# Performance work log

Hardware: AMD Instinct MI355X
Metric: run time of the kernel (lower is better)

Reference implementation:

```python
import jax, jax.numpy as jnp
import numpy as np

T, S, N, E, H, FF = 1024, 2048, 4, 1024, 16, 4096
HD = E // H
EPS = 1e-5


def layer_norm(x, g, b):
    mu = jnp.mean(x, axis=-1, keepdims=True)
    var = jnp.mean(jnp.square(x - mu), axis=-1, keepdims=True)
    return (x - mu) / jnp.sqrt(var + EPS) * g + b


def mha(q_in, k_in, v_in, w_in, b_in, w_out, b_out):
    # q_in: (T,N,E), k_in/v_in: (S,N,E); matches torch F.linear with (3E,E) weight
    t, n, e = q_in.shape
    s = k_in.shape[0]
    wq, wk, wv = jnp.split(w_in, 3, axis=0)
    bq, bk, bv = jnp.split(b_in, 3)
    q = (q_in @ wq.T + bq) * (HD ** -0.5)
    k = k_in @ wk.T + bk
    v = v_in @ wv.T + bv
    # (L,N,E) -> (N*H, L, HD)
    q = q.reshape(t, n * H, HD).transpose(1, 0, 2)
    k = k.reshape(s, n * H, HD).transpose(1, 0, 2)
    v = v.reshape(s, n * H, HD).transpose(1, 0, 2)
    attn = jax.nn.softmax(jnp.einsum('bth,bsh->bts', q, k), axis=-1)
    out = jnp.einsum('bts,bsh->bth', attn, v)  # (N*H, T, HD)
    out = out.transpose(1, 0, 2).reshape(t, n, e)
    return out @ w_out.T + b_out


def setup_inputs() -> dict:
    key = jax.random.key(0)
    ks = jax.random.split(key, 16)
    p = lambda k, shape: jax.random.normal(k, shape, dtype=jnp.float32) * 0.02
    return {
        'tgt': jax.random.normal(ks[0], (T, N, E), dtype=jnp.float32),
        'memory': jax.random.normal(ks[1], (S, N, E), dtype=jnp.float32),
        'sa_w_in': p(ks[2], (3 * E, E)), 'sa_b_in': jnp.zeros((3 * E,), jnp.float32),
        'sa_w_out': p(ks[3], (E, E)), 'sa_b_out': jnp.zeros((E,), jnp.float32),
        'ca_w_in': p(ks[4], (3 * E, E)), 'ca_b_in': jnp.zeros((3 * E,), jnp.float32),
        'ca_w_out': p(ks[5], (E, E)), 'ca_b_out': jnp.zeros((E,), jnp.float32),
        'w1': p(ks[6], (FF, E)), 'b1': jnp.zeros((FF,), jnp.float32),
        'w2': p(ks[7], (E, FF)), 'b2': jnp.zeros((E,), jnp.float32),
        'ln1_g': jnp.ones((E,), jnp.float32), 'ln1_b': jnp.zeros((E,), jnp.float32),
        'ln2_g': jnp.ones((E,), jnp.float32), 'ln2_b': jnp.zeros((E,), jnp.float32),
        'ln3_g': jnp.ones((E,), jnp.float32), 'ln3_b': jnp.zeros((E,), jnp.float32),
    }


def reference(tgt, memory, sa_w_in, sa_b_in, sa_w_out, sa_b_out,
              ca_w_in, ca_b_in, ca_w_out, ca_b_out,
              w1, b1, w2, b2, ln1_g, ln1_b, ln2_g, ln2_b, ln3_g, ln3_b):
    # self-attention block (post-LN residual); dropout = identity (eval mode)
    tgt2 = mha(tgt, tgt, tgt, sa_w_in, sa_b_in, sa_w_out, sa_b_out)
    x = layer_norm(tgt + tgt2, ln1_g, ln1_b)
    # cross-attention block
    tgt2 = mha(x, memory, memory, ca_w_in, ca_b_in, ca_w_out, ca_b_out)
    x = layer_norm(x + tgt2, ln2_g, ln2_b)
    # FFN with relu
    tgt2 = jax.nn.relu(x @ w1.T + b1) @ w2.T + b2
    return layer_norm(x + tgt2, ln3_g, ln3_b)
```

## Files before the change

kernel.cpp:

```cpp
#include <hip/hip_runtime.h>


typedef __bf16 bf16x8 __attribute__((ext_vector_type(8)));
typedef float  f32x4  __attribute__((ext_vector_type(4)));
typedef float  f32x16 __attribute__((ext_vector_type(16)));

#define T_  1024
#define S_  2048
#define NB_ 4
#define E_  1024
#define H_  16
#define HD_ 64
#define FF_ 4096
#define M1_ (T_*NB_)
#define M2_ (S_*NB_)
#define LOG2E 1.44269504088896f

__device__ __forceinline__ unsigned short f2bf(float f){
  unsigned int u = __builtin_bit_cast(unsigned int, f);
  u += 0x7fffu + ((u>>16)&1u);
  return (unsigned short)(u>>16);
}
__device__ __forceinline__ float bf2f(unsigned short h){
  unsigned int u = ((unsigned int)h)<<16;
  return __builtin_bit_cast(float, u);
}

__device__ __forceinline__ void gload16(unsigned short* l, const unsigned short* g){
  __builtin_amdgcn_global_load_lds(
      (const __attribute__((address_space(1))) unsigned int*)g,
      (__attribute__((address_space(3))) unsigned int*)l, 16, 0, 0);
}

__device__ __forceinline__ void perm32swap(unsigned &a, unsigned &b){
  asm("v_permlane32_swap_b32 %0, %1" : "+v"(a), "+v"(b));
}

__device__ __forceinline__ int loff(int row, int kc){
  return ((row>>1)<<6) + (((((row&1)<<2)|kc) ^ ((row>>1)&7))<<3);
}

struct CvtSeg { const float* s; unsigned short* d; int n4; };
struct CvtArgs { CvtSeg seg[8]; int blk_end[8]; };
__global__ __launch_bounds__(256) void f2b_multi_k(CvtArgs a){
  const int b = blockIdx.x;
  int si = 0;
  #pragma unroll
  for (int i=0;i<8;i++) if (b >= a.blk_end[i]) si = i+1;
  const int base = si ? a.blk_end[si-1] : 0;
  const int i4 = (b - base)*256 + threadIdx.x;
  if (i4 >= a.seg[si].n4) return;
  float4 f = ((const float4*)a.seg[si].s)[i4];
  union { unsigned short u[4]; uint2 v; } t;
  t.u[0]=f2bf(f.x); t.u[1]=f2bf(f.y); t.u[2]=f2bf(f.z); t.u[3]=f2bf(f.w);
  ((uint2*)a.seg[si].d)[i4] = t.v;
}

template<int FLAGS, int EPI>
__global__ __launch_bounds__(512, 2) void gemm8_k(
    const unsigned short* __restrict__ A, int lda,
    const unsigned short* __restrict__ B, int ldb,
    const float* __restrict__ bias,
    unsigned short* __restrict__ Cb,
    unsigned short* __restrict__ kb, unsigned short* __restrict__ vtb,
    int M, int N, int K, int Lkv, int nk)
{
  __shared__ unsigned short smem[2][4][256*32];
  const int tid  = threadIdx.x;
  const int wave = tid>>6, lane = tid&63;
  const int l15 = lane&15, l4 = lane>>4;

  int bid = blockIdx.x;
  if ((gridDim.x & 7) == 0){ const int cpx = gridDim.x>>3; bid = (bid&7)*cpx + (bid>>3); }
  const int nbm = M>>8;
  const int bm = bid % nbm, bn = bid / nbm;
  const int brow = bm<<8, bcol = bn<<8;
  const int wm0 = (wave>>2)*128, wn = (wave&3)*64;
  const int NT = K>>5;

  int ldsl[2]; const unsigned short* pA[2]; const unsigned short* pB[2];
  #pragma unroll
  for (int i=0;i<2;i++){
    const int l = i*512 + wave*64 + lane;
    const int grp = l>>3, sl = (l&7) ^ (grp&7);
    const int row = (grp<<1)|(sl>>2), c = sl&3;
    ldsl[i] = l<<3;
    pA[i] = A + (size_t)(brow + row)*lda + (c<<3);
    pB[i] = B + (size_t)(bcol + row)*ldb + (c<<3);
  }

  f32x4 acc[8][4] = {};

  auto stageA = [&](int t){
    unsigned short* s = smem[0][t&3];
    #pragma unroll
    for (int i=0;i<2;i++) gload16(&s[ldsl[i]], pA[i] + t*32);
  };
  auto stageB = [&](int t){
    unsigned short* s = smem[1][t&3];
    #pragma unroll
    for (int i=0;i<2;i++) gload16(&s[ldsl[i]], pB[i] + t*32);
  };

  stageA(0); stageB(0); stageA(1); stageB(1); stageA(2); stageB(2);
  asm volatile("s_waitcnt vmcnt(8)" ::: "memory");
  __builtin_amdgcn_s_barrier();

  for (int t=0; t<NT; ++t){
    const unsigned short* as = smem[0][t&3];
    const unsigned short* bs = smem[1][t&3];
    const bool pre = (t+3 < NT);

    if (pre) stageA(t+3);
    bf16x8 bf[4], af[4];
    #pragma unroll
    for (int n=0;n<4;n++) bf[n] = *(const bf16x8*)&bs[loff(wn + n*16 + l15, l4)];
    #pragma unroll
    for (int m=0;m<4;m++) af[m] = *(const bf16x8*)&as[loff(wm0 + m*16 + l15, l4)];
    __builtin_amdgcn_s_barrier();
    __builtin_amdgcn_s_setprio(1);
    #pragma unroll
    for (int m=0;m<4;m++)
      #pragma unroll
      for (int n=0;n<4;n++)
        acc[m][n] = __builtin_amdgcn_mfma_f32_16x16x32_bf16(af[m], bf[n], acc[m][n], 0,0,0);
    __builtin_amdgcn_s_setprio(0);
    __builtin_amdgcn_s_barrier();

    if (pre) stageB(t+3);
    #pragma unroll
    for (int m=0;m<4;m++) af[m] = *(const bf16x8*)&as[loff(wm0 + 64 + m*16 + l15, l4)];
    __builtin_amdgcn_s_barrier();
    __builtin_amdgcn_s_setprio(1);
    #pragma unroll
    for (int m=0;m<4;m++)
      #pragma unroll
      for (int n=0;n<4;n++)
        acc[4+m][n] = __builtin_amdgcn_mfma_f32_16x16x32_bf16(af[m], bf[n], acc[4+m][n], 0,0,0);
    __builtin_amdgcn_s_setprio(0);
    if (pre)            asm volatile("s_waitcnt vmcnt(8)" ::: "memory");
    else if (t+2 < NT)  asm volatile("s_waitcnt vmcnt(4)" ::: "memory");
    else                asm volatile("s_waitcnt vmcnt(0)" ::: "memory");
    __builtin_amdgcn_s_barrier();
  }

  if constexpr (EPI == 0){
    #pragma unroll
    for (int mi=0;mi<8;mi++){
      #pragma unroll
      for (int r=0;r<4;r++){
        const int rr = brow + wm0 + mi*16 + l4*4 + r;
        #pragma unroll
        for (int n=0;n<4;n++){
          const int cc = bcol + wn + n*16 + l15;
          float v = acc[mi][n][r] + bias[cc];
          if (FLAGS & 1) v = fmaxf(v, 0.f);
          Cb[(size_t)rr*N + cc] = f2bf(v);
        }
      }
    }
  } else {
    if (bcol < nk){
      #pragma unroll
      for (int mi=0;mi<8;mi++){
        #pragma unroll
        for (int r=0;r<4;r++){
          const int rr = brow + wm0 + mi*16 + l4*4 + r;
          const int t = rr>>2, nn = rr&3;
          #pragma unroll
          for (int n=0;n<4;n++){
            const int cc = bcol + wn + n*16 + l15;
            const int h = cc>>6, d = cc&63;
            kb[((size_t)(nn*H_ + h)*Lkv + t)*HD_ + d] = f2bf(acc[mi][n][r] + bias[cc]);
          }
        }
      }
    } else {
      unsigned short* cT = &smem[0][0][0];
      #pragma unroll
      for (int mi=0;mi<8;mi++){
        const int tl = (wm0>>2) + mi*4 + l4;
        #pragma unroll
        for (int n=0;n<4;n++){
          const int ccl = wn + n*16 + l15;
          const float bi = bias[bcol + ccl];
          #pragma unroll
          for (int r=0;r<4;r++){
            const int unit = r*8 + (tl>>3);
            cT[ccl*256 + ((unit ^ (ccl&7))<<3) + (tl&7)] = f2bf(acc[mi][n][r] + bi);
          }
        }
      }
      __syncthreads();
      const int t0 = brow>>2;
      #pragma unroll
      for (int i=0;i<16;i++){
        const int ch = i*512 + tid;
        const int tl8 = ch&7, nn = (ch>>3)&3, ccl = ch>>5;
        const int e = bcol - nk + ccl, h = e>>6, d = e&63;
        const int unit = (nn<<3) | tl8;
        const uint2 v = *(const uint2*)&cT[ccl*256 + ((unit ^ (ccl&7))<<3)];
        *(uint2*)(vtb + ((size_t)(nn*H_ + h)*HD_ + d)*Lkv + t0 + tl8*8) = v;
      }
    }
  }
}

template<int FLAGS, int BN>
__global__ __launch_bounds__(256) void gemm_k(
    const unsigned short* __restrict__ A, int lda,
    const unsigned short* __restrict__ B, int ldb,
    const float* __restrict__ bias,
    const float* __restrict__ res,
    unsigned short* __restrict__ Cb, float* __restrict__ Cf,
    int M, int N, int K)
{
  constexpr int NW = BN/32;
  __shared__ unsigned short a_sh[128*64];
  __shared__ unsigned short b_sh[BN*64];
  const int tid  = threadIdx.x;
  const int wave = tid>>6;
  const int lane = tid&63;
  const int l15 = lane&15, l4 = lane>>4;
  const int row0 = blockIdx.x*128, col0 = blockIdx.y*BN;
  const int wm = (wave>>1)*64, wn = (wave&1)*(BN/2);

  const int lrow = tid>>3;
  const int scol = ((tid&7) ^ (lrow&7)) << 3;
  const int dst8 = (tid&7) << 3;

  f32x4 acc[4][NW] = {};

  for (int k0=0; k0<K; k0+=64){
    const unsigned short* ga = A + (size_t)(row0+lrow)*lda + k0 + scol;
    const unsigned short* gb = B + (size_t)(col0+lrow)*ldb + k0 + scol;
    #pragma unroll
    for (int i=0;i<4;i++)
      gload16(&a_sh[(lrow + i*32)*64 + dst8], ga + (size_t)(i*32)*lda);
    #pragma unroll
    for (int i=0;i<BN/32;i++)
      gload16(&b_sh[(lrow + i*32)*64 + dst8], gb + (size_t)(i*32)*ldb);
    __syncthreads();
    #pragma unroll
    for (int kk=0;kk<2;kk++){
      const int sw = (((kk<<2)|l4) ^ (l15&7)) << 3;
      bf16x8 af[4], bfr[NW];
      #pragma unroll
      for (int m=0;m<4;m++)  af[m]  = *(const bf16x8*)&a_sh[(wm + m*16 + l15)*64 + sw];
      #pragma unroll
      for (int n=0;n<NW;n++) bfr[n] = *(const bf16x8*)&b_sh[(wn + n*16 + l15)*64 + sw];
      #pragma unroll
      for (int m=0;m<4;m++)
        #pragma unroll
        for (int n=0;n<NW;n++)
          acc[m][n] = __builtin_amdgcn_mfma_f32_16x16x32_bf16(af[m], bfr[n], acc[m][n], 0,0,0);
    }
    __syncthreads();
  }

  #pragma unroll
  for (int m=0;m<4;m++){
    #pragma unroll
    for (int r=0;r<4;r++){
      const int rr = row0 + wm + m*16 + l4*4 + r;
      #pragma unroll
      for (int n=0;n<NW;n++){
        const int cc = col0 + wn + n*16 + l15;
        float v = acc[m][n][r] + bias[cc];
        if (FLAGS & 1) v = fmaxf(v, 0.f);
        if (FLAGS & 2) v += res[(size_t)rr*N + cc];
        if (FLAGS & 4) Cb[(size_t)rr*N + cc] = f2bf(v);
        if (FLAGS & 8) Cf[(size_t)rr*N + cc] = v;
      }
    }
  }
}

template<int BN>
__global__ __launch_bounds__(256) void gemm_splitk_k(
    const unsigned short* __restrict__ A, int lda,
    const unsigned short* __restrict__ B, int ldb,
    const float* __restrict__ bias,
    const float* __restrict__ res,
    float* __restrict__ P0, float* __restrict__ P1,
    int M, int N, int K)
{
  constexpr int NW = BN/32;
  __shared__ unsigned short a_sh[128*64];
  __shared__ unsigned short b_sh[BN*64];
  const int tid  = threadIdx.x;
  const int wave = tid>>6;
  const int lane = tid&63;
  const int l15 = lane&15, l4 = lane>>4;
  const int row0 = blockIdx.x*128, col0 = blockIdx.y*BN;
  const int wm = (wave>>1)*64, wn = (wave&1)*(BN/2);
  const int z = blockIdx.z;
  const int kh = K>>1;
  const int kbeg = z*kh;

  const int lrow = tid>>3;
  const int scol = ((tid&7) ^ (lrow&7)) << 3;
  const int dst8 = (tid&7) << 3;

  f32x4 acc[4][NW] = {};

  for (int k0=kbeg; k0<kbeg+kh; k0+=64){
    const unsigned short* ga = A + (size_t)(row0+lrow)*lda + k0 + scol;
    const unsigned short* gb = B + (size_t)(col0+lrow)*ldb + k0 + scol;
    #pragma unroll
    for (int i=0;i<4;i++)
      gload16(&a_sh[(lrow + i*32)*64 + dst8], ga + (size_t)(i*32)*lda);
    #pragma unroll
    for (int i=0;i<BN/32;i++)
      gload16(&b_sh[(lrow + i*32)*64 + dst8], gb + (size_t)(i*32)*ldb);
    __syncthreads();
    #pragma unroll
    for (int kk=0;kk<2;kk++){
      const int sw = (((kk<<2)|l4) ^ (l15&7)) << 3;
      bf16x8 af[4], bfr[NW];
      #pragma unroll
      for (int m=0;m<4;m++)  af[m]  = *(const bf16x8*)&a_sh[(wm + m*16 + l15)*64 + sw];
      #pragma unroll
      for (int n=0;n<NW;n++) bfr[n] = *(const bf16x8*)&b_sh[(wn + n*16 + l15)*64 + sw];
      #pragma unroll
      for (int m=0;m<4;m++)
        #pragma unroll
        for (int n=0;n<NW;n++)
          acc[m][n] = __builtin_amdgcn_mfma_f32_16x16x32_bf16(af[m], bfr[n], acc[m][n], 0,0,0);
    }
    __syncthreads();
  }

  float* out = z ? P1 : P0;
  #pragma unroll
  for (int m=0;m<4;m++){
    #pragma unroll
    for (int r=0;r<4;r++){
      const int rr = row0 + wm + m*16 + l4*4 + r;
      #pragma unroll
      for (int n=0;n<NW;n++){
        const int cc = col0 + wn + n*16 + l15;
        float v = acc[m][n][r];
        if (!z) v += bias[cc] + res[(size_t)rr*N + cc];
        out[(size_t)rr*N + cc] = v;
      }
    }
  }
}

template<int BN>
__global__ __launch_bounds__(256) void gemm_scat_k(
    const unsigned short* __restrict__ A, int lda,
    const unsigned short* __restrict__ B, int ldb,
    const float* __restrict__ bias,
    unsigned short* __restrict__ qb, unsigned short* __restrict__ kb,
    unsigned short* __restrict__ vtb,
    int M, int N, int K, int nq, int nk, int Lq, int Lkv, float qscale)
{
  constexpr int NW = BN/32;
  constexpr int SMEM_ELEMS = (BN==128) ? (128*132) : (128*64 + BN*64);
  __shared__ unsigned short smem[SMEM_ELEMS];
  unsigned short* a_sh = smem;
  unsigned short* b_sh = smem + 128*64;
  const int tid  = threadIdx.x;
  const int wave = tid>>6, lane = tid&63;
  const int l15 = lane&15, l4 = lane>>4;
  const int row0 = blockIdx.x*128, col0 = blockIdx.y*BN;
  const int wm = (wave>>1)*64, wn = (wave&1)*(BN/2);

  const int lrow = tid>>3;
  const int scol = ((tid&7) ^ (lrow&7)) << 3;
  const int dst8 = (tid&7) << 3;

  f32x4 acc[4][NW] = {};

  for (int k0=0; k0<K; k0+=64){
    const unsigned short* ga = A + (size_t)(row0+lrow)*lda + k0 + scol;
    const unsigned short* gb = B + (size_t)(col0+lrow)*ldb + k0 + scol;
    #pragma unroll
    for (int i=0;i<4;i++)
      gload16(&a_sh[(lrow + i*32)*64 + dst8], ga + (size_t)(i*32)*lda);
    #pragma unroll
    for (int i=0;i<BN/32;i++)
      gload16(&b_sh[(lrow + i*32)*64 + dst8], gb + (size_t)(i*32)*ldb);
    __syncthreads();
    #pragma unroll
    for (int kk=0;kk<2;kk++){
      const int sw = (((kk<<2)|l4) ^ (l15&7)) << 3;
      bf16x8 af[4], bfr[NW];
      #pragma unroll
      for (int m=0;m<4;m++)  af[m]  = *(const bf16x8*)&a_sh[(wm + m*16 + l15)*64 + sw];
      #pragma unroll
      for (int n=0;n<NW;n++) bfr[n] = *(const bf16x8*)&b_sh[(wn + n*16 + l15)*64 + sw];
      #pragma unroll
      for (int m=0;m<4;m++)
        #pragma unroll
        for (int n=0;n<NW;n++)
          acc[m][n] = __builtin_amdgcn_mfma_f32_16x16x32_bf16(af[m], bfr[n], acc[m][n], 0,0,0);
    }
    __syncthreads();
  }

  if (col0 < nq + nk){
    const bool isq = (col0 < nq);
    unsigned short* dst = isq ? qb : kb;
    const int  base  = isq ? 0 : nq;
    const int  L     = isq ? Lq : Lkv;
    const float scale = isq ? qscale : 1.0f;
    #pragma unroll
    for (int m=0;m<4;m++){
      #pragma unroll
      for (int r=0;r<4;r++){
        const int rr = row0 + wm + m*16 + l4*4 + r;
        const int t = rr>>2, nn = rr&3;
        #pragma unroll
        for (int n=0;n<NW;n++){
          const int cc = col0 + wn + n*16 + l15;
          const int e = cc - base, h = e>>6, d = e&63;
          const float v = (acc[m][n][r] + bias[cc]) * scale;
          dst[((size_t)(nn*H_ + h)*L + t)*HD_ + d] = f2bf(v);
        }
      }
    }
  } else if constexpr (BN == 128){
    unsigned short* cT = smem;
    #pragma unroll
    for (int m=0;m<4;m++){
      const int tl = ((wm + m*16)>>2) + l4;
      #pragma unroll
      for (int n=0;n<4;n++){
        const int ccl = wn + n*16 + l15;
        const float bi = bias[col0 + ccl];
        #pragma unroll
        for (int r=0;r<4;r++)
          cT[ccl*132 + r*32 + tl] = f2bf(acc[m][n][r] + bi);
      }
    }
    __syncthreads();
    const int t0 = row0>>2;
    const int tl4 = tid&7, c5 = tid>>3;
    const int voff = nq + nk;
    #pragma unroll
    for (int i=0;i<16;i++){
      const int combo = i*32 + c5;
      const int nn = combo&3, ccl = combo>>2;
      const int e = col0 + ccl - voff, h = e>>6, d = e&63;
      const uint2 val = *(const uint2*)&cT[ccl*132 + nn*32 + tl4*4];
      *(uint2*)(vtb + (size_t)((nn*H_ + h)*HD_ + d)*Lkv + t0 + tl4*4) = val;
    }
  }
}

template<bool PARTIAL, int NT>
__global__ __launch_bounds__(256,3) void attn_k(
    const unsigned short* __restrict__ qb, const unsigned short* __restrict__ kb,
    const unsigned short* __restrict__ vtb,
    unsigned short* __restrict__ o_out, float* __restrict__ l_out,
    int T, int S)
{
  static_assert((NT & 1) == 0 && NT >= 4, "NT even");
  __shared__ unsigned short k_sh[2][64*64];
  __shared__ unsigned short v_sh[2][64*64];
  __shared__ float bc_sh[4][32];
  const int tid  = threadIdx.x;
  const int wave = tid>>6, lane = tid&63;
  const int l31  = lane&31;
  const int hv   = lane>>5;
  const int bh   = blockIdx.x;
  const int z    = blockIdx.z;
  const int s_begin = z * (NT*64);
  const int q0   = blockIdx.y*128 + wave*32;
  const size_t qbase = (size_t)bh*T*HD_;
  const size_t kbase = (size_t)bh*S*HD_;
  const size_t vbase = (size_t)bh*HD_*S;

  const int strow = tid>>3;
  const int stch  = tid&7;
  const int sc_sw = (stch ^ (strow&7)) << 3;
  const int dst8  = stch<<3;
  const unsigned short* gk0 = kb  + kbase + (size_t)s_begin*HD_;
  const unsigned short* gv0 = vtb + vbase + s_begin;

  auto stageK = [&](int t, int slot){
    const unsigned short* g = gk0 + (size_t)(t*64)*HD_;
    gload16(&k_sh[slot][(strow   )*64 + dst8], g + (size_t)(strow   )*HD_ + sc_sw);
    gload16(&k_sh[slot][(strow+32)*64 + dst8], g + (size_t)(strow+32)*HD_ + sc_sw);
  };
  auto stageV = [&](int t, int slot){
    const unsigned short* g = gv0 + t*64;
    gload16(&v_sh[slot][(strow   )*64 + dst8], g + (size_t)(strow   )*S + sc_sw);
    gload16(&v_sh[slot][(strow+32)*64 + dst8], g + (size_t)(strow+32)*S + sc_sw);
  };

  bf16x8 qf[4];
  #pragma unroll
  for (int p=0;p<4;p++)
    qf[p] = *(const bf16x8*)(qb + qbase + (size_t)(q0 + l31)*HD_ + p*16 + hv*8);
  asm volatile("" ::: "memory");

  stageK(0, 0);

  f32x16 o0 = {}, o1 = {};
  float rsa = 0.f, rsb = 0.f;
  bf16x8 paA[4], paB[4];

  auto QK = [&](const unsigned short* ksh, f32x16& s0, f32x16& s1){
    #pragma unroll
    for (int p=0;p<4;p++){
      const int slot = 2*p + hv;
      bf16x8 kf0 = *(const bf16x8*)&ksh[(l31     )*64 + ((slot ^ (l31&7))<<3)];
      bf16x8 kf1 = *(const bf16x8*)&ksh[(l31 + 32)*64 + ((slot ^ (l31&7))<<3)];
      s0 = __builtin_amdgcn_mfma_f32_32x32x16_bf16(kf0, qf[p], s0, 0,0,0);
      s1 = __builtin_amdgcn_mfma_f32_32x32x16_bf16(kf1, qf[p], s1, 0,0,0);
    }
  };
  auto PV = [&](const unsigned short* vsh, const bf16x8* pa){
    #pragma unroll
    for (int ks=0;ks<4;ks++){
      const int slot = 2*ks + hv;
      bf16x8 vf0 = *(const bf16x8*)&vsh[(l31     )*64 + ((slot ^ (l31&7))<<3)];
      bf16x8 vf1 = *(const bf16x8*)&vsh[(l31 + 32)*64 + ((slot ^ (l31&7))<<3)];
      o0 = __builtin_amdgcn_mfma_f32_32x32x16_bf16(pa[ks], vf0, o0, 0,0,0);
      o1 = __builtin_amdgcn_mfma_f32_32x32x16_bf16(pa[ks], vf1, o1, 0,0,0);
    }
  };
  auto SM = [&](f32x16& s0, f32x16& s1, bf16x8* pa){
    #pragma unroll
    for (int r=0;r<16;r++){
      s0[r] = __builtin_amdgcn_exp2f(s0[r]);
      s1[r] = __builtin_amdgcn_exp2f(s1[r]);
    }
    #pragma unroll
    for (int r=0;r<16;r+=2){
      rsa += s0[r]   + s1[r];
      rsb += s0[r+1] + s1[r+1];
    }
    #pragma unroll
    for (int ks=0;ks<4;ks++){
      const int base = 8*(ks&1);
      unsigned pkA0, pkA1, pkB0, pkB1;
      if (ks < 2){
        asm("v_cvt_pk_bf16_f32 %0, %1, %2" : "=v"(pkA0) : "v"(s0[base+0]), "v"(s0[base+1]));
        asm("v_cvt_pk_bf16_f32 %0, %1, %2" : "=v"(pkA1) : "v"(s0[base+2]), "v"(s0[base+3]));
        asm("v_cvt_pk_bf16_f32 %0, %1, %2" : "=v"(pkB0) : "v"(s0[base+4]), "v"(s0[base+5]));
        asm("v_cvt_pk_bf16_f32 %0, %1, %2" : "=v"(pkB1) : "v"(s0[base+6]), "v"(s0[base+7]));
      } else {
        asm("v_cvt_pk_bf16_f32 %0, %1, %2" : "=v"(pkA0) : "v"(s1[base+0]), "v"(s1[base+1]));
        asm("v_cvt_pk_bf16_f32 %0, %1, %2" : "=v"(pkA1) : "v"(s1[base+2]), "v"(s1[base+3]));
        asm("v_cvt_pk_bf16_f32 %0, %1, %2" : "=v"(pkB0) : "v"(s1[base+4]), "v"(s1[base+5]));
        asm("v_cvt_pk_bf16_f32 %0, %1, %2" : "=v"(pkB1) : "v"(s1[base+6]), "v"(s1[base+7]));
      }
      perm32swap(pkA0, pkB0);
      perm32swap(pkA1, pkB1);
      union { unsigned w[4]; bf16x8 v; } u;
      u.w[0] = pkA0; u.w[1] = pkA1; u.w[2] = pkB0; u.w[3] = pkB1;
      pa[ks] = u.v;
    }
  };

  {
    stageK(1, 1);
    stageV(0, 0);
    asm volatile("s_waitcnt vmcnt(4)" ::: "memory");
    __builtin_amdgcn_s_barrier();
    f32x16 s0 = {}, s1 = {};
    __builtin_amdgcn_s_setprio(1);
    QK(k_sh[0], s0, s1);
    __builtin_amdgcn_s_setprio(0);
    SM(s0, s1, paA);
    __builtin_amdgcn_s_barrier();
  }

  auto BODY = [&](int i, const bf16x8* paPrev, bf16x8* paCur){
    const int kt = (i+1 < NT) ? (i+1) : (NT-1);
    stageK(kt, (i+1)&1);
    stageV(i, i&1);
    asm volatile("s_waitcnt vmcnt(4)" ::: "memory");
    __builtin_amdgcn_s_barrier();
    f32x16 s0 = {}, s1 = {};
    __builtin_amdgcn_s_setprio(1);
    QK(k_sh[i&1], s0, s1);
    PV(v_sh[(i+1)&1], paPrev);
    __builtin_amdgcn_s_setprio(0);
    SM(s0, s1, paCur);
    __builtin_amdgcn_s_barrier();
  };

  for (int ii=1; ii+1<NT; ii+=2){
    BODY(ii,   paA, paB);
    BODY(ii+1, paB, paA);
  }
  BODY(NT-1, paA, paB);

  asm volatile("s_waitcnt vmcnt(0)" ::: "memory");
  __builtin_amdgcn_s_barrier();
  __builtin_amdgcn_s_setprio(1);
  PV(v_sh[(NT-1)&1], paB);
  __builtin_amdgcn_s_setprio(0);

  float l_run = rsa + rsb;
  {
    unsigned a_ = __builtin_bit_cast(unsigned, l_run), b_ = a_;
    perm32swap(a_, b_);
    l_run += __builtin_bit_cast(float, hv ? a_ : b_);
  }

  if constexpr (PARTIAL){
    const size_t obase = (size_t)(z*64 + bh)*T;
    #pragma unroll
    for (int r=0;r<16;r++){
      const int qr = (r&3) + 8*(r>>2) + 4*hv;
      unsigned short* op = o_out + (obase + q0 + qr)*HD_;
      op[l31]      = f2bf(o0[r]);
      op[l31 + 32] = f2bf(o1[r]);
    }
    if (hv == 0) l_out[obase + q0 + l31] = l_run;
  } else {
    bc_sh[wave][l31] = 1.f / l_run;
    const int nb = bh>>4, hh = bh&15;
    #pragma unroll
    for (int r=0;r<16;r++){
      const int qr  = (r&3) + 8*(r>>2) + 4*hv;
      const float inv = bc_sh[wave][qr];
      const int t = q0 + qr;
      unsigned short* op = o_out + ((size_t)t*NB_ + nb)*E_ + hh*HD_;
      op[l31]      = f2bf(o0[r]*inv);
      op[l31 + 32] = f2bf(o1[r]*inv);
    }
  }
}

__global__ __launch_bounds__(256) void comb_k(
    const unsigned short* __restrict__ opart, const float* __restrict__ lpart,
    unsigned short* __restrict__ outb, int T)
{
  const int bh = blockIdx.y;
  const int t  = blockIdx.x*4 + (threadIdx.x>>6);
  const int d  = threadIdx.x&63;
  const size_t half = (size_t)64*T;
  const size_t row  = (size_t)bh*T + t;
  const float o = bf2f(opart[row*HD_ + d]) + bf2f(opart[(half + row)*HD_ + d]);
  const float l = lpart[row] + lpart[half + row];
  const int nb = bh>>4, hh = bh&15;
  outb[((size_t)t*NB_ + nb)*E_ + hh*HD_ + d] = f2bf(o / l);
}

__global__ __launch_bounds__(256) void ln_k(
    const float* __restrict__ p0, const float* __restrict__ p1,
    const float* __restrict__ g, const float* __restrict__ bb,
    float* __restrict__ of, unsigned short* __restrict__ ob)
{
  const int row = blockIdx.x, tid = threadIdx.x;
  const size_t base = (size_t)row*E_;
  float v[4];
  #pragma unroll
  for (int i=0;i<4;i++){
    const int col = tid + 256*i;
    v[i] = p0[base + col] + p1[base + col];
  }
  float s  = v[0]+v[1]+v[2]+v[3];
  float s2 = v[0]*v[0]+v[1]*v[1]+v[2]*v[2]+v[3]*v[3];
  #pragma unroll
  for (int off=32; off>0; off>>=1){
    s  += __shfl_down(s, off);
    s2 += __shfl_down(s2, off);
  }
  __shared__ float red[8];
  if ((tid&63)==0){ red[tid>>6] = s; red[4+(tid>>6)] = s2; }
  __syncthreads();
  s  = red[0]+red[1]+red[2]+red[3];
  s2 = red[4]+red[5]+red[6]+red[7];
  const float mu   = s * (1.f/E_);
  const float var  = s2 * (1.f/E_) - mu*mu;
  const float rstd = rsqrtf(var + 1e-5f);
  #pragma unroll
  for (int i=0;i<4;i++){
    const int col = tid + 256*i;
    const float y = (v[i]-mu)*rstd*g[col] + bb[col];
    if (of) of[base + col] = y;
    if (ob) ob[base + col] = f2bf(y);
  }
}

extern "C" void kernel_launch(void* const* d_in, const int* in_sizes, int n_in,
                              void* d_out, int out_size, void* d_ws, size_t ws_size,
                              hipStream_t stream)
{
  const float* tgt      = (const float*)d_in[0];
  const float* mem      = (const float*)d_in[1];
  const float* sa_w_in  = (const float*)d_in[2];
  const float* sa_b_in  = (const float*)d_in[3];
  const float* sa_w_out = (const float*)d_in[4];
  const float* sa_b_out = (const float*)d_in[5];
  const float* ca_w_in  = (const float*)d_in[6];
  const float* ca_b_in  = (const float*)d_in[7];
  const float* ca_w_out = (const float*)d_in[8];
  const float* ca_b_out = (const float*)d_in[9];
  const float* w1 = (const float*)d_in[10];
  const float* b1 = (const float*)d_in[11];
  const float* w2 = (const float*)d_in[12];
  const float* b2 = (const float*)d_in[13];
  const float* ln1_g=(const float*)d_in[14]; const float* ln1_b=(const float*)d_in[15];
  const float* ln2_g=(const float*)d_in[16]; const float* ln2_b=(const float*)d_in[17];
  const float* ln3_g=(const float*)d_in[18]; const float* ln3_b=(const float*)d_in[19];

  char* ws = (char*)d_ws;
  size_t off = 0;
  auto alloc = [&](size_t bytes)->char* {
    char* p = ws + off; off += (bytes + 255) & ~(size_t)255; return p;
  };
  unsigned short* w_sa_in_b  = (unsigned short*)alloc((size_t)3*E_*E_*2);
  unsigned short* w_sa_out_b = (unsigned short*)alloc((size_t)E_*E_*2);
  unsigned short* w_ca_in_b  = (unsigned short*)alloc((size_t)3*E_*E_*2);
  unsigned short* w_ca_out_b = (unsigned short*)alloc((size_t)E_*E_*2);
  unsigned short* w1_b  = (unsigned short*)alloc((size_t)FF_*E_*2);
  unsigned short* w2_b  = (unsigned short*)alloc((size_t)E_*FF_*2);
  unsigned short* tgt_b = (unsigned short*)alloc((size_t)M1_*E_*2);
  unsigned short* mem_b = (unsigned short*)alloc((size_t)M2_*E_*2);
  unsigned short* qbuf  = (unsigned short*)alloc((size_t)64*T_*HD_*2);
  unsigned short* kbuf  = (unsigned short*)alloc((size_t)64*S_*HD_*2);
  unsigned short* vtbuf = (unsigned short*)alloc((size_t)64*S_*HD_*2);
  unsigned short* cbuf  = (unsigned short*)alloc((size_t)M1_*FF_*2);
  unsigned short* atto  = (unsigned short*)alloc((size_t)M1_*E_*2);
  unsigned short* opart = (unsigned short*)alloc((size_t)2*64*T_*HD_*2);
  float*          lpart = (float*)alloc((size_t)2*64*T_*4);
  float* resf = (float*)alloc((size_t)M1_*E_*4);
  float* xf   = (float*)alloc((size_t)M1_*E_*4);
  unsigned short* xb = (unsigned short*)alloc((size_t)M1_*E_*2);
  (void)ws_size; (void)in_sizes; (void)n_in; (void)out_size;

  float* P1 = (float*)opart;

  const float QSCALE = 0.125f * LOG2E;

  {
    CvtArgs a;
    const float* srcs[8] = {tgt, mem, sa_w_in, sa_w_out, ca_w_in, ca_w_out, w1, w2};
    unsigned short* dsts[8] = {tgt_b, mem_b, w_sa_in_b, w_sa_out_b, w_ca_in_b, w_ca_out_b, w1_b, w2_b};
    size_t ns[8] = {(size_t)M1_*E_, (size_t)M2_*E_, (size_t)3*E_*E_, (size_t)E_*E_,
                    (size_t)3*E_*E_, (size_t)E_*E_, (size_t)FF_*E_, (size_t)E_*FF_};
    int blk = 0;
    for (int i=0;i<8;i++){
      a.seg[i].s = srcs[i]; a.seg[i].d = dsts[i]; a.seg[i].n4 = (int)(ns[i]/4);
      blk += (a.seg[i].n4 + 255)/256;
      a.blk_end[i] = blk;
    }
    f2b_multi_k<<<blk, 256, 0, stream>>>(a);
  }

  gemm_scat_k<128><<<dim3(M1_/128, (3*E_)/128), 256, 0, stream>>>(
      tgt_b, E_, w_sa_in_b, E_, sa_b_in, qbuf, kbuf, vtbuf,
      M1_, 3*E_, E_, E_, E_, T_, T_, QSCALE);
  attn_k<false,16><<<dim3(64, T_/128, 1), 256, 0, stream>>>(
      qbuf, kbuf, vtbuf, atto, nullptr, T_, T_);
  gemm_splitk_k<64><<<dim3(M1_/128, E_/64, 2), 256, 0, stream>>>(
      atto, E_, w_sa_out_b, E_, sa_b_out, tgt, resf, P1, M1_, E_, E_);
  ln_k<<<M1_, 256, 0, stream>>>(resf, P1, ln1_g, ln1_b, xf, xb);

  gemm8_k<0,1><<<(M2_/256)*((2*E_)/256), 512, 0, stream>>>(
      mem_b, E_, w_ca_in_b + (size_t)E_*E_, E_, ca_b_in + E_, nullptr,
      kbuf, vtbuf, M2_, 2*E_, E_, S_, E_);
  gemm_scat_k<64><<<dim3(M1_/128, E_/64), 256, 0, stream>>>(
      xb, E_, w_ca_in_b, E_, ca_b_in, qbuf, nullptr, nullptr,
      M1_, E_, E_, E_, 0, T_, S_, QSCALE);
  attn_k<true,16><<<dim3(64, T_/128, 2), 256, 0, stream>>>(
      qbuf, kbuf, vtbuf, opart, lpart, T_, S_);
  comb_k<<<dim3(T_/4, 64), 256, 0, stream>>>(opart, lpart, atto, T_);
  gemm_splitk_k<64><<<dim3(M1_/128, E_/64, 2), 256, 0, stream>>>(
      atto, E_, w_ca_out_b, E_, ca_b_out, xf, resf, P1, M1_, E_, E_);
  ln_k<<<M1_, 256, 0, stream>>>(resf, P1, ln2_g, ln2_b, xf, xb);

  gemm8_k<5,0><<<(M1_/256)*(FF_/256), 512, 0, stream>>>(
      xb, E_, w1_b, E_, b1, cbuf, nullptr, nullptr, M1_, FF_, E_, 0, 0);
  gemm_splitk_k<64><<<dim3(M1_/128, E_/64, 2), 256, 0, stream>>>(
      cbuf, FF_, w2_b, FF_, b2, xf, resf, P1, M1_, E_, FF_);
  ln_k<<<M1_, 256, 0, stream>>>(resf, P1, ln3_g, ln3_b, (float*)d_out, nullptr);
}
```

Measured before the change: 378.8 us.

## Route self-attn QKV and FFN2 through 256x256 gemm8 kernel with 4-way split-K

Extends the large-tile gemm8 kernel with a Q/K/V scatter epilogue that applies the query scale, and adds a split-K epilogue writing four fp32 partials. The self-attention QKV projection and the FFN down-projection (K=4096) now use the 256x256 tiled, 4-stage pipelined kernel instead of the smaller 128-tile kernels, aiming for more reuse per tile and better MFMA utilisation. The V-transpose store is widened to 16-byte writes. Partials P2/P3 reuse the kbuf/vtbuf buffers, and LayerNorm now sums four partials, which adds extra fp32 traffic.

```diff
diff --git a/kernel.cpp b/kernel.cpp
--- a/kernel.cpp
+++ b/kernel.cpp
@@ -62,8 +62,13 @@
     const unsigned short* __restrict__ B, int ldb,
     const float* __restrict__ bias,
     unsigned short* __restrict__ Cb,
-    unsigned short* __restrict__ kb, unsigned short* __restrict__ vtb,
-    int M, int N, int K, int Lkv, int nk)
+    unsigned short* __restrict__ qb, unsigned short* __restrict__ kb,
+    unsigned short* __restrict__ vtb,
+    const float* __restrict__ res,
+    float* __restrict__ P0, float* __restrict__ P1f,
+    float* __restrict__ P2, float* __restrict__ P3,
+    int M, int N, int K,
+    int nq, int nk, int Lq, int Lkv, float qscale)
 {
   __shared__ unsigned short smem[2][4][256*32];
   const int tid  = threadIdx.x;
@@ -76,7 +81,10 @@
   const int bm = bid % nbm, bn = bid / nbm;
   const int brow = bm<<8, bcol = bn<<8;
   const int wm0 = (wave>>2)*128, wn = (wave&3)*64;
-  const int NT = K>>5;
+  const int z   = (EPI==2) ? (int)blockIdx.z : 0;
+  const int kh  = (EPI==2) ? (K / (int)gridDim.z) : K;
+  const int kbeg = z * kh;
+  const int NT  = kh>>5;
 
   int ldsl[2]; const unsigned short* pA[2]; const unsigned short* pB[2];
   #pragma unroll
@@ -85,8 +93,8 @@
     const int grp = l>>3, sl = (l&7) ^ (grp&7);
     const int row = (grp<<1)|(sl>>2), c = sl&3;
     ldsl[i] = l<<3;
-    pA[i] = A + (size_t)(brow + row)*lda + (c<<3);
-    pB[i] = B + (size_t)(bcol + row)*ldb + (c<<3);
+    pA[i] = A + (size_t)(brow + row)*lda + kbeg + (c<<3);
+    pB[i] = B + (size_t)(bcol + row)*ldb + kbeg + (c<<3);
   }
 
   f32x4 acc[8][4] = {};
@@ -159,8 +167,14 @@
         }
       }
     }
-  } else {
-    if (bcol < nk){
+  } else if constexpr (EPI == 1){
+    const int voff = nq + nk;
+    if (bcol < voff){
+      const bool isq = (bcol < nq);
+      unsigned short* dst = isq ? qb : kb;
+      const int  base  = isq ? 0 : nq;
+      const int  L     = isq ? Lq : Lkv;
+      const float scale = isq ? qscale : 1.0f;
       #pragma unroll
       for (int mi=0;mi<8;mi++){
         #pragma unroll
@@ -170,8 +184,8 @@
           #pragma unroll
           for (int n=0;n<4;n++){
             const int cc = bcol + wn + n*16 + l15;
-            const int h = cc>>6, d = cc&63;
-            kb[((size_t)(nn*H_ + h)*Lkv + t)*HD_ + d] = f2bf(acc[mi][n][r] + bias[cc]);
+            const int e = cc - base, h = e>>6, d = e&63;
+            dst[((size_t)(nn*H_ + h)*L + t)*HD_ + d] = f2bf((acc[mi][n][r] + bias[cc])*scale);
           }
         }
       }
@@ -197,80 +211,26 @@
       for (int i=0;i<16;i++){
         const int ch = i*512 + tid;
         const int tl8 = ch&7, nn = (ch>>3)&3, ccl = ch>>5;
-        const int e = bcol - nk + ccl, h = e>>6, d = e&63;
+        const int e = bcol - voff + ccl, h = e>>6, d = e&63;
         const int unit = (nn<<3) | tl8;
-        const uint2 v = *(const uint2*)&cT[ccl*256 + ((unit ^ (ccl&7))<<3)];
-        *(uint2*)(vtb + ((size_t)(nn*H_ + h)*HD_ + d)*Lkv + t0 + tl8*8) = v;
+        const uint4 v = *(const uint4*)&cT[ccl*256 + ((unit ^ (ccl&7))<<3)];
+        *(uint4*)(vtb + ((size_t)(nn*H_ + h)*HD_ + d)*Lkv + t0 + tl8*8) = v;
       }
     }
-  }
-}
-
-template<int FLAGS, int BN>
-__global__ __launch_bounds__(256) void gemm_k(
-    const unsigned short* __restrict__ A, int lda,
-    const unsigned short* __restrict__ B, int ldb,
-    const float* __restrict__ bias,
-    const float* __restrict__ res,
-    unsigned short* __restrict__ Cb, float* __restrict__ Cf,
-    int M, int N, int K)
-{
-  constexpr int NW = BN/32;
-  __shared__ unsigned short a_sh[128*64];
-  __shared__ unsigned short b_sh[BN*64];
-  const int tid  = threadIdx.x;
-  const int wave = tid>>6;
-  const int lane = tid&63;
-  const int l15 = lane&15, l4 = lane>>4;
-  const int row0 = blockIdx.x*128, col0 = blockIdx.y*BN;
-  const int wm = (wave>>1)*64, wn = (wave&1)*(BN/2);
-
-  const int lrow = tid>>3;
-  const int scol = ((tid&7) ^ (lrow&7)) << 3;
-  const int dst8 = (tid&7) << 3;
-
-  f32x4 acc[4][NW] = {};
-
-  for (int k0=0; k0<K; k0+=64){
-    const unsigned short* ga = A + (size_t)(row0+lrow)*lda + k0 + scol;
-    const unsigned short* gb = B + (size_t)(col0+lrow)*ldb + k0 + scol;
-    #pragma unroll
-    for (int i=0;i<4;i++)
-      gload16(&a_sh[(lrow + i*32)*64 + dst8], ga + (size_t)(i*32)*lda);
-    #pragma unroll
-    for (int i=0;i<BN/32;i++)
-      gload16(&b_sh[(lrow + i*32)*64 + dst8], gb + (size_t)(i*32)*ldb);
-    __syncthreads();
-    #pragma unroll
-    for (int kk=0;kk<2;kk++){
-      const int sw = (((kk<<2)|l4) ^ (l15&7)) << 3;
-      bf16x8 af[4], bfr[NW];
-      #pragma unroll
-      for (int m=0;m<4;m++)  af[m]  = *(const bf16x8*)&a_sh[(wm + m*16 + l15)*64 + sw];
-      #pragma unroll
-      for (int n=0;n<NW;n++) bfr[n] = *(const bf16x8*)&b_sh[(wn + n*16 + l15)*64 + sw];
-      #pragma unroll
-      for (int m=0;m<4;m++)
+  } else {
+    float* out = (z==0) ? P0 : (z==1) ? P1f : (z==2) ? P2 : P3;
+    #pragma unroll
+    for (int mi=0;mi<8;mi++){
+      #pragma unroll
+      for (int r=0;r<4;r++){
+        const int rr = brow + wm0 + mi*16 + l4*4 + r;
         #pragma unroll
-        for (int n=0;n<NW;n++)
-          acc[m][n] = __builtin_amdgcn_mfma_f32_16x16x32_bf16(af[m], bfr[n], acc[m][n], 0,0,0);
-    }
-    __syncthreads();
-  }
-
-  #pragma unroll
-  for (int m=0;m<4;m++){
-    #pragma unroll
-    for (int r=0;r<4;r++){
-      const int rr = row0 + wm + m*16 + l4*4 + r;
-      #pragma unroll
-      for (int n=0;n<NW;n++){
-        const int cc = col0 + wn + n*16 + l15;
-        float v = acc[m][n][r] + bias[cc];
-        if (FLAGS & 1) v = fmaxf(v, 0.f);
-        if (FLAGS & 2) v += res[(size_t)rr*N + cc];
-        if (FLAGS & 4) Cb[(size_t)rr*N + cc] = f2bf(v);
-        if (FLAGS & 8) Cf[(size_t)rr*N + cc] = v;
+        for (int n=0;n<4;n++){
+          const int cc = bcol + wn + n*16 + l15;
+          float v = acc[mi][n][r];
+          if (z == 0) v += bias[cc] + res[(size_t)rr*N + cc];
+          out[(size_t)rr*N + cc] = v;
+        }
       }
     }
   }
@@ -421,32 +381,6 @@
           dst[((size_t)(nn*H_ + h)*L + t)*HD_ + d] = f2bf(v);
         }
       }
-    }
-  } else if constexpr (BN == 128){
-    unsigned short* cT = smem;
-    #pragma unroll
-    for (int m=0;m<4;m++){
-      const int tl = ((wm + m*16)>>2) + l4;
-      #pragma unroll
-      for (int n=0;n<4;n++){
-        const int ccl = wn + n*16 + l15;
-        const float bi = bias[col0 + ccl];
-        #pragma unroll
-        for (int r=0;r<4;r++)
-          cT[ccl*132 + r*32 + tl] = f2bf(acc[m][n][r] + bi);
-      }
-    }
-    __syncthreads();
-    const int t0 = row0>>2;
-    const int tl4 = tid&7, c5 = tid>>3;
-    const int voff = nq + nk;
-    #pragma unroll
-    for (int i=0;i<16;i++){
-      const int combo = i*32 + c5;
-      const int nn = combo&3, ccl = combo>>2;
-      const int e = col0 + ccl - voff, h = e>>6, d = e&63;
-      const uint2 val = *(const uint2*)&cT[ccl*132 + nn*32 + tl4*4];
-      *(uint2*)(vtb + (size_t)((nn*H_ + h)*HD_ + d)*Lkv + t0 + tl4*4) = val;
     }
   }
 }
@@ -647,6 +581,7 @@
 
 __global__ __launch_bounds__(256) void ln_k(
     const float* __restrict__ p0, const float* __restrict__ p1,
+    const float* __restrict__ p2, const float* __restrict__ p3,
     const float* __restrict__ g, const float* __restrict__ bb,
     float* __restrict__ of, unsigned short* __restrict__ ob)
 {
@@ -657,6 +592,8 @@
   for (int i=0;i<4;i++){
     const int col = tid + 256*i;
     v[i] = p0[base + col] + p1[base + col];
+    if (p2) v[i] += p2[base + col];
+    if (p3) v[i] += p3[base + col];
   }
   float s  = v[0]+v[1]+v[2]+v[3];
   float s2 = v[0]*v[0]+v[1]*v[1]+v[2]*v[2]+v[3]*v[3];
@@ -730,6 +667,8 @@
   (void)ws_size; (void)in_sizes; (void)n_in; (void)out_size;
 
   float* P1 = (float*)opart;
+  float* P2 = (float*)kbuf;
+  float* P3 = (float*)vtbuf;
 
   const float QSCALE = 0.125f * LOG2E;
 
@@ -748,18 +687,21 @@
     f2b_multi_k<<<blk, 256, 0, stream>>>(a);
   }
 
-  gemm_scat_k<128><<<dim3(M1_/128, (3*E_)/128), 256, 0, stream>>>(
-      tgt_b, E_, w_sa_in_b, E_, sa_b_in, qbuf, kbuf, vtbuf,
+  gemm8_k<0,1><<<(M1_/256)*((3*E_)/256), 512, 0, stream>>>(
+      tgt_b, E_, w_sa_in_b, E_, sa_b_in, nullptr, qbuf, kbuf, vtbuf,
+      nullptr, nullptr, nullptr, nullptr, nullptr,
       M1_, 3*E_, E_, E_, E_, T_, T_, QSCALE);
   attn_k<false,16><<<dim3(64, T_/128, 1), 256, 0, stream>>>(
       qbuf, kbuf, vtbuf, atto, nullptr, T_, T_);
   gemm_splitk_k<64><<<dim3(M1_/128, E_/64, 2), 256, 0, stream>>>(
       atto, E_, w_sa_out_b, E_, sa_b_out, tgt, resf, P1, M1_, E_, E_);
-  ln_k<<<M1_, 256, 0, stream>>>(resf, P1, ln1_g, ln1_b, xf, xb);
+  ln_k<<<M1_, 256, 0, stream>>>(resf, P1, nullptr, nullptr, ln1_g, ln1_b, xf, xb);
 
   gemm8_k<0,1><<<(M2_/256)*((2*E_)/256), 512, 0, stream>>>(
       mem_b, E_, w_ca_in_b + (size_t)E_*E_, E_, ca_b_in + E_, nullptr,
-      kbuf, vtbuf, M2_, 2*E_, E_, S_, E_);
+      nullptr, kbuf, vtbuf,
+      nullptr, nullptr, nullptr, nullptr, nullptr,
+      M2_, 2*E_, E_, 0, E_, S_, S_, QSCALE);
   gemm_scat_k<64><<<dim3(M1_/128, E_/64), 256, 0, stream>>>(
       xb, E_, w_ca_in_b, E_, ca_b_in, qbuf, nullptr, nullptr,
       M1_, E_, E_, E_, 0, T_, S_, QSCALE);
@@ -768,11 +710,15 @@
   comb_k<<<dim3(T_/4, 64), 256, 0, stream>>>(opart, lpart, atto, T_);
   gemm_splitk_k<64><<<dim3(M1_/128, E_/64, 2), 256, 0, stream>>>(
       atto, E_, w_ca_out_b, E_, ca_b_out, xf, resf, P1, M1_, E_, E_);
-  ln_k<<<M1_, 256, 0, stream>>>(resf, P1, ln2_g, ln2_b, xf, xb);
+  ln_k<<<M1_, 256, 0, stream>>>(resf, P1, nullptr, nullptr, ln2_g, ln2_b, xf, xb);
 
   gemm8_k<5,0><<<(M1_/256)*(FF_/256), 512, 0, stream>>>(
-      xb, E_, w1_b, E_, b1, cbuf, nullptr, nullptr, M1_, FF_, E_, 0, 0);
-  gemm_splitk_k<64><<<dim3(M1_/128, E_/64, 2), 256, 0, stream>>>(
-      cbuf, FF_, w2_b, FF_, b2, xf, resf, P1, M1_, E_, FF_);
-  ln_k<<<M1_, 256, 0, stream>>>(resf, P1, ln3_g, ln3_b, (float*)d_out, nullptr);
-}
+      xb, E_, w1_b, E_, b1, cbuf, nullptr, nullptr, nullptr,
+      nullptr, nullptr, nullptr, nullptr, nullptr,
+      M1_, FF_, E_, 0, 0, 0, 0, 0.f);
+  gemm8_k<0,2><<<dim3((M1_/256)*(E_/256), 1, 4), 512, 0, stream>>>(
+      cbuf, FF_, w2_b, FF_, b2, nullptr, nullptr, nullptr, nullptr,
+      xf, resf, P1, P2, P3,
+      M1_, E_, FF_, 0, 0, 0, 0, 0.f);
+  ln_k<<<M1_, 256, 0, stream>>>(resf, P1, P2, P3, ln3_g, ln3_b, (float*)d_out, nullptr);
+}
```

Result: slower. 406.0 us (+7.2%).
